# Performance work log

Measured on AMD Instinct MI355X. Metric: run time of the kernel, lower is better.

The kernel has to match this reference:

```python
import jax, jax.numpy as jnp
import numpy as np

ROUTINGS = 3

def squash(v, axis=-1):
    # scale = |v|^2 / (1+|v|^2) / (|v| + 1e-8)
    norm = jnp.linalg.norm(v, axis=axis, keepdims=True)
    scale = norm ** 2 / (1.0 + norm ** 2) / (norm + 1e-8)
    return scale * v

def setup_inputs() -> dict:
    key = jax.random.key(0)
    k1, k2 = jax.random.split(key)
    B, IN_N, IN_D, OUT_N, OUT_D = 32, 2048, 16, 64, 32
    x = jax.random.normal(k1, (B, IN_N, IN_D), dtype=jnp.float32)
    weight = 0.01 * jax.random.normal(k2, (OUT_N, IN_N, OUT_D, IN_D), dtype=jnp.float32)
    return {"x": x, "weight": weight}

def reference(x, weight):
    # x: [B, in_n, in_d]; weight: [out_n, in_n, out_d, in_d]
    # x_hat: [B, out_n, in_n, out_d]
    x_hat = jnp.einsum('oidk,bik->boid', weight, x)
    B, out_n, in_n, _ = x_hat.shape
    b = jnp.zeros((B, out_n, in_n), dtype=x_hat.dtype)
    # note: original code sets x_hat_detached = x_hat with no detach, so same tensor everywhere
    outputs = None
    for i in range(ROUTINGS):
        c = jax.nn.softmax(b, axis=1)                      # softmax over out_n
        s = jnp.einsum('boi,boid->bod', c, x_hat)[:, :, None, :]  # [B, out_n, 1, out_d]
        outputs = squash(s, axis=-1)
        if i != ROUTINGS - 1:
            b = b + jnp.einsum('bojd,boid->boi', outputs, x_hat)
    return jnp.squeeze(outputs, axis=-2)                   # [B, out_n, out_d]
```

## Files before the change

### kernel.cpp

```cpp
#include <hip/hip_runtime.h>
#include <cstdint>

typedef __attribute__((ext_vector_type(8))) short short8;
typedef __attribute__((ext_vector_type(16))) float f32x16;

#define B_   32
#define IN_  2048
#define ID_  16
#define ON_  64
#define OD_  32

__device__ __forceinline__ unsigned short f2bf(float f) {
    union { float f; uint32_t u; } c; c.f = f;
    uint32_t u = c.u;
    uint32_t r = (u + 0x7FFFu + ((u >> 16) & 1u)) >> 16;
    return (unsigned short)r;
}
__device__ __forceinline__ unsigned int pack2(float a, float b) {
    return (unsigned int)f2bf(a) | ((unsigned int)f2bf(b) << 16);
}


__global__ __launch_bounds__(256) void xconv_k(
    const float* __restrict__ x, uint4* __restrict__ xbf)
{
    int t = threadIdx.x, lane = t & 63, wv = t >> 6;
    int i = blockIdx.x * 4 + wv;
    int b = lane & 31, half = lane >> 5;
    const float* g = x + ((size_t)b * IN_ + i) * ID_ + half * 8;
    float4 a = *(const float4*)g;
    float4 c = *(const float4*)(g + 4);
    uint4 p = { pack2(a.x, a.y), pack2(a.z, a.w), pack2(c.x, c.y), pack2(c.z, c.w) };
    xbf[(size_t)i * 64 + lane] = p;
}

__global__ __launch_bounds__(256) void pass0_k2(
    const float* __restrict__ w, const uint4* __restrict__ xbf,
    uint4* __restrict__ wbf, float* __restrict__ part)
{
    int t = threadIdx.x, lane = t & 63, wv = t >> 6;
    int og = blockIdx.x & 15, ic = blockIdx.x >> 4;
    int o = og * 4 + wv;
    int d = lane & 31, half = lane >> 5;

    f32x16 acc = {};
    #pragma unroll 4
    for (int ii = 0; ii < 32; ++ii) {
        int i = ic * 32 + ii;
        union { uint4 u; short8 s; } af;
        af.u = xbf[(size_t)i * 64 + lane];
        const float* g = w + ((size_t)o * IN_ + i) * 512 + d * 16 + half * 8;
        float4 a = *(const float4*)g;
        float4 c = *(const float4*)(g + 4);
        union { uint4 u; short8 s; } bf;
        bf.u = (uint4){ pack2(a.x, a.y), pack2(a.z, a.w), pack2(c.x, c.y), pack2(c.z, c.w) };
        wbf[((size_t)o * IN_ + i) * 64 + lane] = bf.u;
        acc = __builtin_amdgcn_mfma_f32_32x32x16_bf16(af.s, bf.s, acc, 0, 0, 0);
    }
    float* dst = part + (size_t)ic * 65536;
    #pragma unroll
    for (int r = 0; r < 16; ++r) {
        int b = (r & 3) + 8 * (r >> 2) + 4 * half;
        dst[(size_t)b * 2048 + o * 32 + d] = acc[r];
    }
}

__global__ __launch_bounds__(256, 4) void logits_raw_k(
    const uint4* __restrict__ wbf, const uint4* __restrict__ xbf,
    const float* __restrict__ vin , float* __restrict__ L)
{
    int t = threadIdx.x, lane = t & 63, wv = t >> 6;
    int o = blockIdx.x & 63, ic = blockIdx.x >> 6;
    int b = lane & 31, half = lane >> 5;

    float vr[16];
    #pragma unroll
    for (int r = 0; r < 16; ++r) {
        int d = (r & 3) + 8 * (r >> 2) + 4 * half;
        vr[r] = vin[(size_t)o * (B_ * OD_) + b * 32 + d];
    }

    #pragma unroll 8
    for (int ii = 0; ii < 8; ++ii) {
        int i = ic * 32 + wv * 8 + ii;
        union { uint4 u; short8 s; } af, bb;
        af.u = xbf[(size_t)i * 64 + lane];
        bb.u = wbf[((size_t)o * IN_ + i) * 64 + lane];
        f32x16 z = {};
        f32x16 C2 = __builtin_amdgcn_mfma_f32_32x32x16_bf16(bb.s, af.s, z, 0, 0, 0);
        float p0 = C2[0] * vr[0], p1 = C2[1] * vr[1];
        float p2 = C2[2] * vr[2], p3 = C2[3] * vr[3];
        #pragma unroll
        for (int r = 4; r < 16; r += 4) {
            p0 += C2[r + 0] * vr[r + 0];
            p1 += C2[r + 1] * vr[r + 1];
            p2 += C2[r + 2] * vr[r + 2];
            p3 += C2[r + 3] * vr[r + 3];
        }
        float partial = (p0 + p1) + (p2 + p3);
        float total = partial + __shfl_xor(partial, 32);
        if (half == 0)
            L[((size_t)i * 64 + o) * 32 + b] = total;
    }
}

__global__ __launch_bounds__(256) void msum_k(
    const float* __restrict__ L, float* __restrict__ msum )
{
    __shared__ float sl[4][2048];
    int t = threadIdx.x, lane = t & 63, wv = t >> 6;
    int i = blockIdx.x * 4 + wv;
    const float4* src4 = reinterpret_cast<const float4*>(L + (size_t)i * 2048);
    float4* dst4 = reinterpret_cast<float4*>(sl[wv]);
    #pragma unroll
    for (int j = 0; j < 8; ++j) dst4[j * 64 + lane] = src4[j * 64 + lane];
    int b = lane & 31, half = lane >> 5;
    float m = -1e30f;
    #pragma unroll
    for (int o = 0; o < 32; ++o)
        m = fmaxf(m, sl[wv][(half * 32 + o) * 32 + b]);
    m = fmaxf(m, __shfl_xor(m, 32));
    float s = 0.0f;
    #pragma unroll
    for (int o = 0; o < 32; ++o)
        s += __expf(sl[wv][(half * 32 + o) * 32 + b] - m);
    s += __shfl_xor(s, 32);
    if (half == 0) {
        msum[(size_t)i * 64 + b]      = m;
        msum[(size_t)i * 64 + 32 + b] = 1.0f / s;
    }
}

__global__ __launch_bounds__(256, 4) void accum_k(
    const uint4* __restrict__ wbf, const uint4* __restrict__ xbf,
    const float* __restrict__ L, const float* __restrict__ msum,
    float* __restrict__ part)
{
    int t = threadIdx.x, lane = t & 63, wv = t >> 6;
    int o = blockIdx.x & 63, ic = blockIdx.x >> 6;
    int d = lane & 31, half = lane >> 5;
    int b = lane & 31;
    int i0 = ic * 128 + wv * 32;

    f32x16 acc = {};
    #pragma unroll 8
    for (int ii = 0; ii < 32; ++ii) {
        int i = i0 + ii;
        union { uint4 u; short8 s; } af;
        af.u = xbf[(size_t)i * 64 + lane];
        union { uint4 u; short8 s; } bb;
        bb.u = wbf[((size_t)o * IN_ + i) * 64 + lane];
        float Lv   = L[((size_t)i * 64 + o) * 32 + b];
        float mv   = msum[(size_t)i * 64 + b];
        float rinv = msum[(size_t)i * 64 + 32 + b];
        float cl = __expf(Lv - mv) * rinv;
        union { uint4 u; short8 s; } afs;
        #pragma unroll
        for (int j = 0; j < 4; ++j) {
            uint32_t p = ((const uint32_t*)&af.u)[j];
            union { float f; uint32_t u; } lo, hi;
            lo.u = (p & 0xFFFFu) << 16;
            hi.u = p & 0xFFFF0000u;
            ((uint32_t*)&afs.u)[j] = pack2(lo.f * cl, hi.f * cl);
        }
        acc = __builtin_amdgcn_mfma_f32_32x32x16_bf16(afs.s, bb.s, acc, 0, 0, 0);
    }

    float* dst = part + (size_t)(ic * 4 + wv) * 65536;
    #pragma unroll
    for (int r = 0; r < 16; ++r) {
        int bb2 = (r & 3) + 8 * (r >> 2) + 4 * half;
        dst[(size_t)bb2 * 2048 + o * 32 + d] = acc[r];
    }
}

__global__ __launch_bounds__(256) void reduce_squash_k(
    const float* __restrict__ part, int nslices, float scale,
    const float* __restrict__ addprev, float* __restrict__ outv, int out_bod)
{
    int t = threadIdx.x, lane = t & 63, wv = t >> 6;
    int row = blockIdx.x * 8 + wv * 2 + (lane >> 5);
    int d = lane & 31;
    const float* p = part + (size_t)row * 32 + d;
    float s0 = 0, s1 = 0, s2 = 0, s3 = 0, s4 = 0, s5 = 0, s6 = 0, s7 = 0;
    for (int s = 0; s < nslices; s += 8) {
        s0 += p[(size_t)(s + 0) * 65536];
        s1 += p[(size_t)(s + 1) * 65536];
        s2 += p[(size_t)(s + 2) * 65536];
        s3 += p[(size_t)(s + 3) * 65536];
        s4 += p[(size_t)(s + 4) * 65536];
        s5 += p[(size_t)(s + 5) * 65536];
        s6 += p[(size_t)(s + 6) * 65536];
        s7 += p[(size_t)(s + 7) * 65536];
    }
    float sv = (((s0 + s1) + (s2 + s3)) + ((s4 + s5) + (s6 + s7))) * scale;
    float n2 = sv * sv;
    #pragma unroll
    for (int m = 1; m <= 16; m <<= 1) n2 += __shfl_xor(n2, m, 32);
    float norm = sqrtf(n2);
    float sc = n2 / ((1.0f + n2) * (norm + 1e-8f));
    float v = sc * sv;
    int b = row >> 6, o = row & 63;
    if (addprev) v += addprev[((size_t)o * B_ + b) * OD_ + d];
    if (out_bod) outv[(size_t)row * OD_ + d] = v;
    else         outv[((size_t)o * B_ + b) * OD_ + d] = v;
}


__global__ __launch_bounds__(256, 4) void pass0_k(
    const float* __restrict__ x, const float* __restrict__ w, float* __restrict__ S)
{
    __shared__ __align__(16) unsigned short lw[16 * 512];
    __shared__ __align__(16) unsigned short lx[512];

    const int t = threadIdx.x, lane = t & 63, wv = t >> 6;
    const int bx = blockIdx.x;
    const int ic = bx & 255, og = bx >> 8;
    const int o0 = og * 16;
    const int d = lane & 31, half = lane >> 5;

    f32x16 acc[4] = {};

    for (int i = ic * 8; i < ic * 8 + 8; ++i) {
        #pragma unroll
        for (int r = 0; r < 4; ++r) {
            int cidx = r * 256 + t;
            int ol = cidx >> 6, j8 = cidx & 63;
            const float* g = w + (size_t)(o0 + ol) * 1048576 + (size_t)i * 512 + j8 * 8;
            float4 a = *(const float4*)g;
            float4 b2 = *(const float4*)(g + 4);
            uint4 val = { pack2(a.x, a.y), pack2(a.z, a.w), pack2(b2.x, b2.y), pack2(b2.z, b2.w) };
            *reinterpret_cast<uint4*>(&lw[ol * 512 + j8 * 8]) = val;
        }
        if (t < 128) {
            int b = t >> 2, kq = t & 3;
            float4 a = *(const float4*)(x + ((size_t)b * IN_ + i) * ID_ + kq * 4);
            uint2 val = { pack2(a.x, a.y), pack2(a.z, a.w) };
            *reinterpret_cast<uint2*>(&lx[b * 16 + kq * 4]) = val;
        }
        __syncthreads();

        short8 afr = *reinterpret_cast<const short8*>(&lx[(lane & 31) * 16 + half * 8]);
        #pragma unroll
        for (int oi = 0; oi < 4; ++oi) {
            int ol = wv * 4 + oi;
            short8 bfr = *reinterpret_cast<const short8*>(&lw[ol * 512 + d * 16 + half * 8]);
            acc[oi] = __builtin_amdgcn_mfma_f32_32x32x16_bf16(afr, bfr, acc[oi], 0, 0, 0);
        }
        __syncthreads();
    }

    #pragma unroll
    for (int oi = 0; oi < 4; ++oi) {
        int o = o0 + wv * 4 + oi;
        #pragma unroll
        for (int r = 0; r < 16; ++r) {
            int b = (r & 3) + 8 * (r >> 2) + 4 * half;
            atomicAdd(&S[((size_t)b * ON_ + o) * OD_ + d], acc[oi][r]);
        }
    }
}

__global__ __launch_bounds__(512, 2) void pass_route_k(
    const float* __restrict__ x, const float* __restrict__ w,
    const float* __restrict__ vin, float* __restrict__ S)
{
    __shared__ __align__(16) unsigned short lw[64 * 512];
    __shared__ __align__(16) unsigned short lx[512];
    __shared__ float blds[B_ * ON_];
    __shared__ float clds[B_ * ON_];

    const int t = threadIdx.x, lane = t & 63, wv = t >> 6;
    const int ic = blockIdx.x;
    const int d = lane & 31, half = lane >> 5;

    f32x16 acc[8] = {};

    for (int i = ic * 8; i < ic * 8 + 8; ++i) {
        #pragma unroll
        for (int r = 0; r < 8; ++r) {
            int cidx = r * 512 + t;
            int ol = cidx >> 6, j8 = cidx & 63;
            const float* g = w + (size_t)ol * 1048576 + (size_t)i * 512 + j8 * 8;
            float4 a = *(const float4*)g;
            float4 b2 = *(const float4*)(g + 4);
            uint4 val = { pack2(a.x, a.y), pack2(a.z, a.w), pack2(b2.x, b2.y), pack2(b2.z, b2.w) };
            *reinterpret_cast<uint4*>(&lw[ol * 512 + j8 * 8]) = val;
        }
        if (t < 128) {
            int b = t >> 2, kq = t & 3;
            float4 a = *(const float4*)(x + ((size_t)b * IN_ + i) * ID_ + kq * 4);
            uint2 val = { pack2(a.x, a.y), pack2(a.z, a.w) };
            *reinterpret_cast<uint2*>(&lx[b * 16 + kq * 4]) = val;
        }
        __syncthreads();

        short8 afr = *reinterpret_cast<const short8*>(&lx[(lane & 31) * 16 + half * 8]);
        short8 bfr[8];

        #pragma unroll
        for (int oi = 0; oi < 8; ++oi) {
            int o = wv * 8 + oi;
            bfr[oi] = *reinterpret_cast<const short8*>(&lw[o * 512 + d * 16 + half * 8]);
            f32x16 z = {};
            f32x16 C = __builtin_amdgcn_mfma_f32_32x32x16_bf16(afr, bfr[oi], z, 0, 0, 0);
            float bvp[16];
            #pragma unroll
            for (int r = 0; r < 16; ++r) {
                int b = (r & 3) + 8 * (r >> 2) + 4 * half;
                float vv = vin[((size_t)o * B_ + b) * OD_ + d];
                bvp[r] = C[r] * vv;
            }
            #pragma unroll
            for (int m = 1; m <= 16; m <<= 1) {
                #pragma unroll
                for (int r = 0; r < 16; ++r)
                    bvp[r] += __shfl_xor(bvp[r], m, 32);
            }
            if ((lane & 31) == 0) {
                #pragma unroll
                for (int r = 0; r < 16; ++r) {
                    int b = (r & 3) + 8 * (r >> 2) + 4 * half;
                    blds[b * ON_ + o] = bvp[r];
                }
            }
        }
        __syncthreads();

        {
            int o = t & 63, bq = t >> 6;
            #pragma unroll
            for (int j = 0; j < 4; ++j) {
                int b = bq + 8 * j;
                float v = blds[b * ON_ + o];
                float m = v;
                #pragma unroll
                for (int mm = 1; mm <= 32; mm <<= 1) m = fmaxf(m, __shfl_xor(m, mm, 64));
                float e = __expf(v - m);
                float ssum = e;
                #pragma unroll
                for (int mm = 1; mm <= 32; mm <<= 1) ssum += __shfl_xor(ssum, mm, 64);
                clds[b * ON_ + o] = e / ssum;
            }
        }
        __syncthreads();

        #pragma unroll
        for (int oi = 0; oi < 8; ++oi) {
            int o = wv * 8 + oi;
            f32x16 z = {};
            f32x16 C = __builtin_amdgcn_mfma_f32_32x32x16_bf16(afr, bfr[oi], z, 0, 0, 0);
            #pragma unroll
            for (int r = 0; r < 16; ++r) {
                int b = (r & 3) + 8 * (r >> 2) + 4 * half;
                acc[oi][r] += clds[b * ON_ + o] * C[r];
            }
        }
        __syncthreads();
    }

    #pragma unroll
    for (int oi = 0; oi < 8; ++oi) {
        int o = wv * 8 + oi;
        #pragma unroll
        for (int r = 0; r < 16; ++r) {
            int b = (r & 3) + 8 * (r >> 2) + 4 * half;
            atomicAdd(&S[((size_t)b * ON_ + o) * OD_ + d], acc[oi][r]);
        }
    }
}

__global__ __launch_bounds__(256) void squash_k(
    const float* __restrict__ S, const float* __restrict__ addprev,
    float* __restrict__ out, float scale, int out_bod)
{
    int t = threadIdx.x;
    int row = blockIdx.x * 8 + (t >> 5);
    int d = t & 31;
    int b = row >> 6, o = row & 63;
    float s = S[(size_t)row * OD_ + d] * scale;
    float n2 = s * s;
    #pragma unroll
    for (int mm = 1; mm <= 16; mm <<= 1) n2 += __shfl_xor(n2, mm, 32);
    float norm = sqrtf(n2);
    float sc = n2 / ((1.0f + n2) * (norm + 1e-8f));
    float v = sc * s;
    if (addprev) v += addprev[((size_t)o * B_ + b) * OD_ + d];
    if (out_bod)
        out[((size_t)b * ON_ + o) * OD_ + d] = v;
    else
        out[((size_t)o * B_ + b) * OD_ + d] = v;
}


extern "C" void kernel_launch(void* const* d_in, const int* in_sizes, int n_in,
                              void* d_out, int out_size, void* d_ws, size_t ws_size,
                              hipStream_t stream) {
    (void)in_sizes; (void)n_in; (void)out_size;
    const float* x = (const float*)d_in[0];
    const float* w = (const float*)d_in[1];
    float* out = (float*)d_out;

    const size_t WBF_B  = 134217728;
    const size_t XBF_B  = 2097152;
    const size_t PART_B = 16777216;
    const size_t L_B    = 16777216;
    const size_t MS_B   = 524288;
    const size_t V_B    = 262144;
    const size_t NEED   = WBF_B + XBF_B + PART_B + L_B + MS_B + 2 * V_B;

    if (ws_size >= NEED) {
        uint8_t* wsb = (uint8_t*)d_ws;
        uint4* wbf  = (uint4*)wsb;
        uint4* xbf  = (uint4*)(wsb + WBF_B);
        float* part = (float*)(wsb + WBF_B + XBF_B);
        float* Lg   = (float*)(wsb + WBF_B + XBF_B + PART_B);
        float* ms   = (float*)(wsb + WBF_B + XBF_B + PART_B + L_B);
        float* v0   = (float*)(wsb + WBF_B + XBF_B + PART_B + L_B + MS_B);
        float* vsum = (float*)(wsb + WBF_B + XBF_B + PART_B + L_B + MS_B + V_B);

        xconv_k<<<512, 256, 0, stream>>>(x, xbf);
        pass0_k2<<<1024, 256, 0, stream>>>(w, xbf, wbf, part);
        reduce_squash_k<<<256, 256, 0, stream>>>(part, 64, 1.0f / 64.0f, nullptr, v0, 0);

        logits_raw_k<<<4096, 256, 0, stream>>>(wbf, xbf, v0, Lg);
        msum_k<<<512, 256, 0, stream>>>(Lg, ms);
        accum_k<<<1024, 256, 0, stream>>>(wbf, xbf, Lg, ms, part);
        reduce_squash_k<<<256, 256, 0, stream>>>(part, 64, 1.0f, v0, vsum, 0);

        logits_raw_k<<<4096, 256, 0, stream>>>(wbf, xbf, vsum, Lg);
        msum_k<<<512, 256, 0, stream>>>(Lg, ms);
        accum_k<<<1024, 256, 0, stream>>>(wbf, xbf, Lg, ms, part);
        reduce_squash_k<<<256, 256, 0, stream>>>(part, 64, 1.0f, nullptr, out, 1);
    } else {
        float* S    = (float*)d_ws;
        float* v0   = S + 65536;
        float* vsum = v0 + 65536;
        const size_t Sbytes = (size_t)65536 * sizeof(float);

        hipMemsetAsync(S, 0, Sbytes, stream);
        pass0_k<<<1024, 256, 0, stream>>>(x, w, S);
        squash_k<<<256, 256, 0, stream>>>(S, nullptr, v0, 1.0f / 64.0f, 0);

        hipMemsetAsync(S, 0, Sbytes, stream);
        pass_route_k<<<256, 512, 0, stream>>>(x, w, v0, S);
        squash_k<<<256, 256, 0, stream>>>(S, v0, vsum, 1.0f, 0);

        hipMemsetAsync(S, 0, Sbytes, stream);
        pass_route_k<<<256, 512, 0, stream>>>(x, w, vsum, S);
        squash_k<<<256, 256, 0, stream>>>(S, nullptr, out, 1.0f, 1);
    }
}
```

Measured before the change: 251.7 us.

## Apply routing coefficients to MFMA output instead of rescaling bf16 inputs

In accum_k, the per-(b,i) coupling coefficient is no longer folded into the bf16 x operand. Unpacking, scaling and repacking the operand cost VALU work, so the kernel now runs an un-accumulated MFMA and does an FMA of cl*C2 into the fp32 accumulator. This removes the bf16 repacking and its rounding, but adds 16 VALU FMAs per MFMA, and the MFMA no longer accumulates in place. The partial-sum layout becomes d-major with b contiguous, and the reduce+squash is split into an elementwise slice reduction kernel plus a small per-(o,b) squash kernel. logits_raw_k also pairs two input rows so that every lane does a store instead of only half of them.

```diff
diff --git a/kernel.cpp b/kernel.cpp
--- a/kernel.cpp
+++ b/kernel.cpp
@@ -41,7 +41,7 @@
     int t = threadIdx.x, lane = t & 63, wv = t >> 6;
     int og = blockIdx.x & 15, ic = blockIdx.x >> 4;
     int o = og * 4 + wv;
-    int d = lane & 31, half = lane >> 5;
+    int b = lane & 31, half = lane >> 5;
 
     f32x16 acc = {};
     #pragma unroll 4
@@ -49,19 +49,19 @@
         int i = ic * 32 + ii;
         union { uint4 u; short8 s; } af;
         af.u = xbf[(size_t)i * 64 + lane];
-        const float* g = w + ((size_t)o * IN_ + i) * 512 + d * 16 + half * 8;
+        const float* g = w + ((size_t)o * IN_ + i) * 512 + b * 16 + half * 8;
         float4 a = *(const float4*)g;
         float4 c = *(const float4*)(g + 4);
         union { uint4 u; short8 s; } bf;
         bf.u = (uint4){ pack2(a.x, a.y), pack2(a.z, a.w), pack2(c.x, c.y), pack2(c.z, c.w) };
         wbf[((size_t)o * IN_ + i) * 64 + lane] = bf.u;
-        acc = __builtin_amdgcn_mfma_f32_32x32x16_bf16(af.s, bf.s, acc, 0, 0, 0);
+        acc = __builtin_amdgcn_mfma_f32_32x32x16_bf16(bf.s, af.s, acc, 0, 0, 0);
     }
     float* dst = part + (size_t)ic * 65536;
     #pragma unroll
     for (int r = 0; r < 16; ++r) {
-        int b = (r & 3) + 8 * (r >> 2) + 4 * half;
-        dst[(size_t)b * 2048 + o * 32 + d] = acc[r];
+        int d = (r & 3) + 8 * (r >> 2) + 4 * half;
+        dst[(o * 32 + d) * 32 + b] = acc[r];
     }
 }
 
@@ -80,27 +80,31 @@
         vr[r] = vin[(size_t)o * (B_ * OD_) + b * 32 + d];
     }
 
-    #pragma unroll 8
-    for (int ii = 0; ii < 8; ++ii) {
-        int i = ic * 32 + wv * 8 + ii;
-        union { uint4 u; short8 s; } af, bb;
-        af.u = xbf[(size_t)i * 64 + lane];
-        bb.u = wbf[((size_t)o * IN_ + i) * 64 + lane];
-        f32x16 z = {};
-        f32x16 C2 = __builtin_amdgcn_mfma_f32_32x32x16_bf16(bb.s, af.s, z, 0, 0, 0);
-        float p0 = C2[0] * vr[0], p1 = C2[1] * vr[1];
-        float p2 = C2[2] * vr[2], p3 = C2[3] * vr[3];
-        #pragma unroll
-        for (int r = 4; r < 16; r += 4) {
-            p0 += C2[r + 0] * vr[r + 0];
-            p1 += C2[r + 1] * vr[r + 1];
-            p2 += C2[r + 2] * vr[r + 2];
-            p3 += C2[r + 3] * vr[r + 3];
-        }
-        float partial = (p0 + p1) + (p2 + p3);
-        float total = partial + __shfl_xor(partial, 32);
-        if (half == 0)
-            L[((size_t)i * 64 + o) * 32 + b] = total;
+    #pragma unroll
+    for (int ii = 0; ii < 8; ii += 2) {
+        int i0 = ic * 32 + wv * 8 + ii;
+        float tot[2];
+        #pragma unroll
+        for (int q = 0; q < 2; ++q) {
+            union { uint4 u; short8 s; } af, bb;
+            af.u = xbf[(size_t)(i0 + q) * 64 + lane];
+            bb.u = wbf[((size_t)o * IN_ + (i0 + q)) * 64 + lane];
+            f32x16 z = {};
+            f32x16 C2 = __builtin_amdgcn_mfma_f32_32x32x16_bf16(bb.s, af.s, z, 0, 0, 0);
+            float p0 = C2[0] * vr[0], p1 = C2[1] * vr[1];
+            float p2 = C2[2] * vr[2], p3 = C2[3] * vr[3];
+            #pragma unroll
+            for (int r = 4; r < 16; r += 4) {
+                p0 += C2[r + 0] * vr[r + 0];
+                p1 += C2[r + 1] * vr[r + 1];
+                p2 += C2[r + 2] * vr[r + 2];
+                p3 += C2[r + 3] * vr[r + 3];
+            }
+            float partial = (p0 + p1) + (p2 + p3);
+            tot[q] = partial + __shfl_xor(partial, 32);
+        }
+        int it = i0 + half;
+        L[((size_t)it * 64 + o) * 32 + b] = half ? tot[1] : tot[0];
     }
 }
 
@@ -138,52 +142,42 @@
 {
     int t = threadIdx.x, lane = t & 63, wv = t >> 6;
     int o = blockIdx.x & 63, ic = blockIdx.x >> 6;
-    int d = lane & 31, half = lane >> 5;
-    int b = lane & 31;
+    int b = lane & 31, half = lane >> 5;
     int i0 = ic * 128 + wv * 32;
 
     f32x16 acc = {};
     #pragma unroll 8
     for (int ii = 0; ii < 32; ++ii) {
         int i = i0 + ii;
-        union { uint4 u; short8 s; } af;
+        union { uint4 u; short8 s; } af, bb;
         af.u = xbf[(size_t)i * 64 + lane];
-        union { uint4 u; short8 s; } bb;
         bb.u = wbf[((size_t)o * IN_ + i) * 64 + lane];
+        f32x16 z = {};
+        f32x16 C2 = __builtin_amdgcn_mfma_f32_32x32x16_bf16(bb.s, af.s, z, 0, 0, 0);
         float Lv   = L[((size_t)i * 64 + o) * 32 + b];
         float mv   = msum[(size_t)i * 64 + b];
         float rinv = msum[(size_t)i * 64 + 32 + b];
         float cl = __expf(Lv - mv) * rinv;
-        union { uint4 u; short8 s; } afs;
-        #pragma unroll
-        for (int j = 0; j < 4; ++j) {
-            uint32_t p = ((const uint32_t*)&af.u)[j];
-            union { float f; uint32_t u; } lo, hi;
-            lo.u = (p & 0xFFFFu) << 16;
-            hi.u = p & 0xFFFF0000u;
-            ((uint32_t*)&afs.u)[j] = pack2(lo.f * cl, hi.f * cl);
-        }
-        acc = __builtin_amdgcn_mfma_f32_32x32x16_bf16(afs.s, bb.s, acc, 0, 0, 0);
+        #pragma unroll
+        for (int r = 0; r < 16; ++r) acc[r] += cl * C2[r];
     }
 
     float* dst = part + (size_t)(ic * 4 + wv) * 65536;
     #pragma unroll
     for (int r = 0; r < 16; ++r) {
-        int bb2 = (r & 3) + 8 * (r >> 2) + 4 * half;
-        dst[(size_t)bb2 * 2048 + o * 32 + d] = acc[r];
-    }
-}
-
-__global__ __launch_bounds__(256) void reduce_squash_k(
-    const float* __restrict__ part, int nslices, float scale,
-    const float* __restrict__ addprev, float* __restrict__ outv, int out_bod)
-{
-    int t = threadIdx.x, lane = t & 63, wv = t >> 6;
-    int row = blockIdx.x * 8 + wv * 2 + (lane >> 5);
-    int d = lane & 31;
-    const float* p = part + (size_t)row * 32 + d;
+        int d = (r & 3) + 8 * (r >> 2) + 4 * half;
+        dst[(o * 32 + d) * 32 + b] = acc[r];
+    }
+}
+
+__global__ __launch_bounds__(256) void reduceA_k(
+    const float* __restrict__ part, float* __restrict__ Ssum)
+{
+    int idx = blockIdx.x * 256 + threadIdx.x;
+    const float* p = part + idx;
     float s0 = 0, s1 = 0, s2 = 0, s3 = 0, s4 = 0, s5 = 0, s6 = 0, s7 = 0;
-    for (int s = 0; s < nslices; s += 8) {
+    #pragma unroll
+    for (int s = 0; s < 64; s += 8) {
         s0 += p[(size_t)(s + 0) * 65536];
         s1 += p[(size_t)(s + 1) * 65536];
         s2 += p[(size_t)(s + 2) * 65536];
@@ -193,17 +187,37 @@
         s6 += p[(size_t)(s + 6) * 65536];
         s7 += p[(size_t)(s + 7) * 65536];
     }
-    float sv = (((s0 + s1) + (s2 + s3)) + ((s4 + s5) + (s6 + s7))) * scale;
-    float n2 = sv * sv;
-    #pragma unroll
-    for (int m = 1; m <= 16; m <<= 1) n2 += __shfl_xor(n2, m, 32);
+    Ssum[idx] = (((s0 + s1) + (s2 + s3)) + ((s4 + s5) + (s6 + s7)));
+}
+
+__global__ __launch_bounds__(64) void reduceB_k(
+    const float* __restrict__ Ssum, float scale,
+    const float* __restrict__ addprev, float* __restrict__ outv, int out_bod)
+{
+    int lane = threadIdx.x & 63;
+    int b = lane & 31;
+    int o = blockIdx.x * 2 + (lane >> 5);
+    float sv[32];
+    float n2 = 0.0f;
+    #pragma unroll
+    for (int d = 0; d < 32; ++d) {
+        float v = Ssum[(o * 32 + d) * 32 + b] * scale;
+        sv[d] = v;
+        n2 += v * v;
+    }
     float norm = sqrtf(n2);
     float sc = n2 / ((1.0f + n2) * (norm + 1e-8f));
-    float v = sc * sv;
-    int b = row >> 6, o = row & 63;
-    if (addprev) v += addprev[((size_t)o * B_ + b) * OD_ + d];
-    if (out_bod) outv[(size_t)row * OD_ + d] = v;
-    else         outv[((size_t)o * B_ + b) * OD_ + d] = v;
+    if (out_bod) {
+        float* dst = outv + ((size_t)b * 64 + o) * 32;
+        #pragma unroll
+        for (int d = 0; d < 32; ++d) dst[d] = sc * sv[d];
+    } else {
+        float* dst = outv + (size_t)o * 1024 + b * 32;
+        const float* pv = addprev ? addprev + (size_t)o * 1024 + b * 32 : nullptr;
+        #pragma unroll
+        for (int d = 0; d < 32; ++d)
+            dst[d] = sc * sv[d] + (pv ? pv[d] : 0.0f);
+    }
 }
 
 
@@ -406,8 +420,9 @@
     const size_t PART_B = 16777216;
     const size_t L_B    = 16777216;
     const size_t MS_B   = 524288;
+    const size_t SS_B   = 262144;
     const size_t V_B    = 262144;
-    const size_t NEED   = WBF_B + XBF_B + PART_B + L_B + MS_B + 2 * V_B;
+    const size_t NEED   = WBF_B + XBF_B + PART_B + L_B + MS_B + SS_B + 2 * V_B;
 
     if (ws_size >= NEED) {
         uint8_t* wsb = (uint8_t*)d_ws;
@@ -416,22 +431,26 @@
         float* part = (float*)(wsb + WBF_B + XBF_B);
         float* Lg   = (float*)(wsb + WBF_B + XBF_B + PART_B);
         float* ms   = (float*)(wsb + WBF_B + XBF_B + PART_B + L_B);
-        float* v0   = (float*)(wsb + WBF_B + XBF_B + PART_B + L_B + MS_B);
-        float* vsum = (float*)(wsb + WBF_B + XBF_B + PART_B + L_B + MS_B + V_B);
+        float* Ss   = (float*)(wsb + WBF_B + XBF_B + PART_B + L_B + MS_B);
+        float* v0   = (float*)(wsb + WBF_B + XBF_B + PART_B + L_B + MS_B + SS_B);
+        float* vsum = (float*)(wsb + WBF_B + XBF_B + PART_B + L_B + MS_B + SS_B + V_B);
 
         xconv_k<<<512, 256, 0, stream>>>(x, xbf);
         pass0_k2<<<1024, 256, 0, stream>>>(w, xbf, wbf, part);
-        reduce_squash_k<<<256, 256, 0, stream>>>(part, 64, 1.0f / 64.0f, nullptr, v0, 0);
+        reduceA_k<<<256, 256, 0, stream>>>(part, Ss);
+        reduceB_k<<<32, 64, 0, stream>>>(Ss, 1.0f / 64.0f, nullptr, v0, 0);
 
         logits_raw_k<<<4096, 256, 0, stream>>>(wbf, xbf, v0, Lg);
         msum_k<<<512, 256, 0, stream>>>(Lg, ms);
         accum_k<<<1024, 256, 0, stream>>>(wbf, xbf, Lg, ms, part);
-        reduce_squash_k<<<256, 256, 0, stream>>>(part, 64, 1.0f, v0, vsum, 0);
+        reduceA_k<<<256, 256, 0, stream>>>(part, Ss);
+        reduceB_k<<<32, 64, 0, stream>>>(Ss, 1.0f, v0, vsum, 0);
 
         logits_raw_k<<<4096, 256, 0, stream>>>(wbf, xbf, vsum, Lg);
         msum_k<<<512, 256, 0, stream>>>(Lg, ms);
         accum_k<<<1024, 256, 0, stream>>>(wbf, xbf, Lg, ms, part);
-        reduce_squash_k<<<256, 256, 0, stream>>>(part, 64, 1.0f, nullptr, out, 1);
+        reduceA_k<<<256, 256, 0, stream>>>(part, Ss);
+        reduceB_k<<<32, 64, 0, stream>>>(Ss, 1.0f, nullptr, out, 1);
     } else {
         float* S    = (float*)d_ws;
         float* v0   = S + 65536;
```

Measured after the change: 260.4 us. 1.03x slower.
